# Optimization experiments

Measured on AMD Instinct MI355X. Metric: run time of the kernel, lower is better.

## Reference

```python
import jax, jax.numpy as jnp
import numpy as np

IMAGE_SIZE = 256
CHUNK = 64            # faces per z-buffer scan step
LIGHT = (0.0, 0.0, 3.0)      # PointLights location
AMBIENT, DIFFUSE, SPECULAR, SHININESS = 0.5, 0.3, 0.2, 64.0  # pytorch3d defaults
EPS = 1e-8


def setup_inputs() -> dict:
    n_lat, n_lon, B = 72, 72, 2
    theta = np.linspace(0.15, np.pi - 0.15, n_lat)
    phi = np.linspace(0.0, 2.0 * np.pi, n_lon, endpoint=False)
    t, p = np.meshgrid(theta, phi, indexing='ij')
    sphere = np.stack([np.sin(t) * np.cos(p), np.cos(t), np.sin(t) * np.sin(p)], -1).reshape(-1, 3)
    idx = np.arange(n_lat * n_lon).reshape(n_lat, n_lon)
    idr = np.roll(idx, -1, axis=1)
    f1 = np.stack([idx[:-1], idx[1:], idr[:-1]], -1).reshape(-1, 3)
    f2 = np.stack([idr[:-1], idx[1:], idr[1:]], -1).reshape(-1, 3)
    faces = np.concatenate([f1, f2], 0).astype(np.int32)  # [10224, 3]
    key = jax.random.key(0)
    radii = 1.0 + 0.05 * jax.random.normal(jax.random.fold_in(key, 1), (B, sphere.shape[0], 1))
    vertices = (jnp.asarray(sphere, jnp.float32)[None] * radii).astype(jnp.float32)  # [B,V,3]
    tm = jnp.tile(jnp.eye(4, dtype=jnp.float32)[None], (B, 1, 1)).at[:, 2, 3].set(4.0)  # R=I, T=(0,0,4)
    focal = jnp.full((B, 1), 300.0, jnp.float32)
    pp = jnp.full((1, 2), IMAGE_SIZE / 2.0, jnp.float32)
    return {'vertices': vertices, 'transform_matrix': tm, 'focal_length': focal,
            'principal_point': pp, 'faces': jnp.asarray(faces)}


def _edge(ax, ay, bx, by, px, py):
    return (bx - ax) * (py - ay) - (by - ay) * (px - ax)


def _gather_tri(attr, f_v):
    # attr [B,V,C], f_v [B,P,3] -> [B,P,3,C]
    return jax.vmap(lambda a, f: a[f])(attr, f_v)


def _normalize(v):
    return v / (jnp.linalg.norm(v, axis=-1, keepdims=True) + EPS)


def _rasterize(verts_pix, faces_chunks, px, py):
    # verts_pix [B,V,3] (x_pix, y_pix, z_view); faces_chunks [n_chunks, CHUNK, 3]
    B, P = verts_pix.shape[0], px.shape[0]
    vp = jax.lax.stop_gradient(verts_pix)  # hard rasterization: face ids are non-differentiable

    def body(carry, inp):
        zbuf, fid = carry
        fchunk, off = inp
        tri = vp[:, fchunk]                      # [B,C,3,3]
        x, y, z = tri[..., 0], tri[..., 1], tri[..., 2]   # [B,C,3]
        pxb, pyb = px[None, None], py[None, None]
        w0 = _edge(x[..., 1, None], y[..., 1, None], x[..., 2, None], y[..., 2, None], pxb, pyb)
        w1 = _edge(x[..., 2, None], y[..., 2, None], x[..., 0, None], y[..., 0, None], pxb, pyb)
        w2 = _edge(x[..., 0, None], y[..., 0, None], x[..., 1, None], y[..., 1, None], pxb, pyb)
        denom = w0 + w1 + w2                     # signed twice-area, [B,C,P]
        safe = jnp.where(jnp.abs(denom) > EPS, denom, 1.0)
        b0, b1, b2 = w0 / safe, w1 / safe, w2 / safe
        zint = b0 * z[..., 0, None] + b1 * z[..., 1, None] + b2 * z[..., 2, None]
        inside = (b0 >= 0) & (b1 >= 0) & (b2 >= 0) & (jnp.abs(denom) > EPS) & (zint > 1e-4)
        zc = jnp.where(inside, zint, jnp.inf)    # [B,C,P]
        j = jnp.argmin(zc, axis=1)               # [B,P]
        best_z = jnp.take_along_axis(zc, j[:, None, :], axis=1)[:, 0]
        upd = best_z < zbuf
        zbuf = jnp.where(upd, best_z, zbuf)
        fid = jnp.where(upd, off + j.astype(jnp.int32), fid)
        return (zbuf, fid), None

    n_chunks = faces_chunks.shape[0]
    offs = (jnp.arange(n_chunks) * CHUNK).astype(jnp.int32)
    init = (jnp.full((B, P), jnp.inf, vp.dtype), jnp.zeros((B, P), jnp.int32))
    (zbuf, fid), _ = jax.lax.scan(body, init, (faces_chunks, offs))
    return zbuf, fid


def _render(vertices, transform_matrix, focal_length, principal_point, faces):
    B, V, _ = vertices.shape
    H = W = IMAGE_SIZE
    P = H * W
    R, T = transform_matrix[:, :3, :3], transform_matrix[:, :3, 3]
    # pytorch3d row-vector convention: X_view = X @ R + T
    vview = jnp.einsum('bvi,bij->bvj', vertices, R) + T[:, None]
    z = vview[..., 2]
    x_pix = focal_length * vview[..., 0] / z + principal_point[:, 0][:, None]
    y_pix = focal_length * vview[..., 1] / z + principal_point[:, 1][:, None]
    verts_pix = jnp.stack([x_pix, y_pix, z], -1)                 # [B,V,3]

    gy, gx = jnp.meshgrid(jnp.arange(H) + 0.5, jnp.arange(W) + 0.5, indexing='ij')
    px, py = gx.reshape(-1).astype(vertices.dtype), gy.reshape(-1).astype(vertices.dtype)

    F = faces.shape[0]
    Fpad = ((F + CHUNK - 1) // CHUNK) * CHUNK
    faces_pad = jnp.pad(faces, ((0, Fpad - F), (0, 0)))          # pad = degenerate (0,0,0)
    zbuf, fid = _rasterize(verts_pix, faces_pad.reshape(-1, CHUNK, 3), px, py)
    valid = jnp.isfinite(zbuf)                                   # [B,P]

    # differentiable re-computation of barycentrics for the winning face
    f_v = faces_pad.reshape(-1, 3)[fid]                          # [B,P,3]
    tp = _gather_tri(verts_pix, f_v)                             # [B,P,3,3]
    xk, yk = tp[..., 0], tp[..., 1]
    w0 = _edge(xk[..., 1], yk[..., 1], xk[..., 2], yk[..., 2], px[None], py[None])
    w1 = _edge(xk[..., 2], yk[..., 2], xk[..., 0], yk[..., 0], px[None], py[None])
    w2 = _edge(xk[..., 0], yk[..., 0], xk[..., 1], yk[..., 1], px[None], py[None])
    denom = w0 + w1 + w2
    safe = jnp.where(jnp.abs(denom) > EPS, denom, 1.0)
    bary = jnp.stack([w0, w1, w2], -1) / safe[..., None]         # [B,P,3]

    # area-weighted vertex normals
    tw = vertices[:, faces]                                      # [B,F,3,3]
    fn = jnp.cross(tw[:, :, 1] - tw[:, :, 0], tw[:, :, 2] - tw[:, :, 0])
    vn = jnp.zeros_like(vertices)
    for k in range(3):
        vn = vn.at[:, faces[:, k]].add(fn)
    vn = _normalize(vn)

    pix_pos = jnp.einsum('bpk,bpkc->bpc', bary, _gather_tri(vertices, f_v))
    pix_n = _normalize(jnp.einsum('bpk,bpkc->bpc', bary, _gather_tri(vn, f_v)))

    cam = -jnp.einsum('bj,bij->bi', T, R)                        # camera center in world
    light = jnp.asarray(LIGHT, vertices.dtype)
    L = _normalize(light - pix_pos)
    Vd = _normalize(cam[:, None] - pix_pos)
    ndl = jnp.sum(pix_n * L, -1)
    refl = 2.0 * ndl[..., None] * pix_n - L
    spec = SPECULAR * jnp.maximum(jnp.sum(refl * Vd, -1), 0.0) ** SHININESS * (ndl > 0)
    col = AMBIENT + DIFFUSE * jnp.maximum(ndl, 0.0) + spec       # white texels -> gray shading
    rgb = jnp.where(valid, col, 1.0)                             # white background
    images = jnp.broadcast_to(rgb[:, None], (B, 3, P)).reshape(B, 3, H, W) * 255.0
    alpha = valid.astype(vertices.dtype).reshape(B, 1, H, W)
    return images, alpha


def reference(vertices, transform_matrix, focal_length, principal_point, faces):
    return _render(vertices, transform_matrix, focal_length, principal_point, faces)
```

## Files before the change

kernel.cpp:

```cpp
#include <hip/hip_runtime.h>
#include <math.h>

#define IMG 256
#define PIX (IMG * IMG)
#define SENT 0xFFFFFFFFFFFFFFFFull


__global__ __launch_bounds__(256) void k_transform(
    const float* __restrict__ verts, const float* __restrict__ tm,
    const float* __restrict__ focal, const float* __restrict__ pp,
    float* __restrict__ vp, float* __restrict__ vn,
    unsigned long long* __restrict__ zpk, int B, int V) {
#pragma clang fp contract(off)
    int idx = blockIdx.x * blockDim.x + threadIdx.x;
    int nthreads = gridDim.x * blockDim.x;
    for (int i = idx; i < B * PIX; i += nthreads) zpk[i] = SENT;
    if (idx >= B * V) return;
    int b = idx / V;
    const float* tmb = tm + b * 16;
    float x = verts[idx * 3 + 0];
    float y = verts[idx * 3 + 1];
    float z = verts[idx * 3 + 2];
    float vv[3];
    for (int j = 0; j < 3; ++j) {
        float s = x * tmb[0 * 4 + j] + y * tmb[1 * 4 + j];
        s = s + z * tmb[2 * 4 + j];
        vv[j] = s + tmb[j * 4 + 3];
    }
    float f = focal[b];
    float xp = (f * vv[0]) / vv[2] + pp[0];
    float yp = (f * vv[1]) / vv[2] + pp[1];
    vp[idx * 3 + 0] = xp;
    vp[idx * 3 + 1] = yp;
    vp[idx * 3 + 2] = vv[2];
    vn[idx * 3 + 0] = 0.0f;
    vn[idx * 3 + 1] = 0.0f;
    vn[idx * 3 + 2] = 0.0f;
}

__global__ __launch_bounds__(256) void k_pack(
    const float* __restrict__ verts, const int* __restrict__ faces,
    const float* __restrict__ vp, float* __restrict__ packed,
    float* __restrict__ vn, int B, int F, int FP, int V) {
#pragma clang fp contract(off)
    int idx = blockIdx.x * blockDim.x + threadIdx.x;
    if (idx >= B * FP) return;
    int b = idx / FP;
    int f = idx - b * FP;
    int i0 = 0, i1 = 0, i2 = 0;
    if (f < F) {
        i0 = faces[f * 3 + 0];
        i1 = faces[f * 3 + 1];
        i2 = faces[f * 3 + 2];
    }
    const float* vpb = vp + (size_t)b * V * 3;
    float* pk = packed + (size_t)idx * 9;
    pk[0] = vpb[i0 * 3 + 0]; pk[1] = vpb[i0 * 3 + 1]; pk[2] = vpb[i0 * 3 + 2];
    pk[3] = vpb[i1 * 3 + 0]; pk[4] = vpb[i1 * 3 + 1]; pk[5] = vpb[i1 * 3 + 2];
    pk[6] = vpb[i2 * 3 + 0]; pk[7] = vpb[i2 * 3 + 1]; pk[8] = vpb[i2 * 3 + 2];
    if (f < F) {
        const float* wv = verts + (size_t)b * V * 3;
        float ax = wv[i1 * 3 + 0] - wv[i0 * 3 + 0];
        float ay = wv[i1 * 3 + 1] - wv[i0 * 3 + 1];
        float az = wv[i1 * 3 + 2] - wv[i0 * 3 + 2];
        float bx = wv[i2 * 3 + 0] - wv[i0 * 3 + 0];
        float by = wv[i2 * 3 + 1] - wv[i0 * 3 + 1];
        float bz = wv[i2 * 3 + 2] - wv[i0 * 3 + 2];
        float fnx = ay * bz - az * by;
        float fny = az * bx - ax * bz;
        float fnz = ax * by - ay * bx;
        float* vnb = vn + (size_t)b * V * 3;
        atomicAdd(&vnb[i0 * 3 + 0], fnx);
        atomicAdd(&vnb[i0 * 3 + 1], fny);
        atomicAdd(&vnb[i0 * 3 + 2], fnz);
        atomicAdd(&vnb[i1 * 3 + 0], fnx);
        atomicAdd(&vnb[i1 * 3 + 1], fny);
        atomicAdd(&vnb[i1 * 3 + 2], fnz);
        atomicAdd(&vnb[i2 * 3 + 0], fnx);
        atomicAdd(&vnb[i2 * 3 + 1], fny);
        atomicAdd(&vnb[i2 * 3 + 2], fnz);
    }
}

__global__ __launch_bounds__(256) void k_raster(
    const float* __restrict__ packed,
    unsigned long long* __restrict__ zpk, int FP) {
#pragma clang fp contract(off)
    int b = blockIdx.y;
    int wid = threadIdx.x >> 6;
    int lane = threadIdx.x & 63;
    int f = blockIdx.x * 4 + wid;
    if (f >= FP) return;

    const float* t = packed + ((size_t)b * FP + f) * 9;
    float x0 = t[0], y0 = t[1], z0 = t[2];
    float x1 = t[3], y1 = t[4], z1 = t[5];
    float x2 = t[6], y2 = t[7], z2 = t[8];

    float xmin = fminf(fminf(x0, x1), x2);
    float xmax = fmaxf(fmaxf(x0, x1), x2);
    float ymin = fminf(fminf(y0, y1), y2);
    float ymax = fmaxf(fmaxf(y0, y1), y2);

    int ix0 = (int)floorf(xmin - 0.5f); ix0 = ix0 < 0 ? 0 : ix0;
    int iy0 = (int)floorf(ymin - 0.5f); iy0 = iy0 < 0 ? 0 : iy0;
    int ix1 = (int)ceilf(xmax - 0.5f);  ix1 = ix1 > IMG - 1 ? IMG - 1 : ix1;
    int iy1 = (int)ceilf(ymax - 0.5f);  iy1 = iy1 > IMG - 1 ? IMG - 1 : iy1;
    int w = ix1 - ix0 + 1;
    int h = iy1 - iy0 + 1;
    if (w <= 0 || h <= 0) return;
    int n = w * h;

    unsigned long long* zb = zpk + (size_t)b * PIX;
    for (int i = lane; i < n; i += 64) {
        int iy = (int)((unsigned)i / (unsigned)w);
        int ix = i - iy * w;
        float px = (float)(ix0 + ix) + 0.5f;
        float py = (float)(iy0 + iy) + 0.5f;
        float w0 = (x2 - x1) * (py - y1) - (y2 - y1) * (px - x1);
        float w1 = (x0 - x2) * (py - y2) - (y0 - y2) * (px - x2);
        float w2 = (x1 - x0) * (py - y0) - (y1 - y0) * (px - x0);
        float denom = (w0 + w1) + w2;
        bool dok = fabsf(denom) > 1e-8f;
        float safe = dok ? denom : 1.0f;
        float b0 = w0 / safe;
        float b1 = w1 / safe;
        float b2 = w2 / safe;
        float zint = (b0 * z0 + b1 * z1) + b2 * z2;
        bool inside = (b0 >= 0.0f) && (b1 >= 0.0f) && (b2 >= 0.0f) &&
                      dok && (zint > 1e-4f);
        if (inside) {
            unsigned long long cand =
                ((unsigned long long)__float_as_uint(zint) << 32) |
                (unsigned int)f;
            atomicMin(&zb[(iy0 + iy) * IMG + (ix0 + ix)], cand);
        }
    }
}

__global__ __launch_bounds__(256) void k_shade(
    const float* __restrict__ verts, const int* __restrict__ faces,
    const float* __restrict__ tm, const float* __restrict__ packed,
    const float* __restrict__ vn, const unsigned long long* __restrict__ zpk,
    float* __restrict__ out, int B, int V, int FP) {
#pragma clang fp contract(off)
    int p = blockIdx.x * blockDim.x + threadIdx.x;
    int b = blockIdx.y;
    if (p >= PIX) return;
    size_t imgbase = (size_t)b * 3 * PIX;
    size_t alphabase = (size_t)B * 3 * PIX + (size_t)b * PIX;
    unsigned long long v = zpk[(size_t)b * PIX + p];
    if (v == SENT) {
        out[imgbase + 0 * PIX + p] = 255.0f;
        out[imgbase + 1 * PIX + p] = 255.0f;
        out[imgbase + 2 * PIX + p] = 255.0f;
        out[alphabase + p] = 0.0f;
        return;
    }
    int f = (int)(v & 0xFFFFFFFFull);
    float px = (float)(p & (IMG - 1)) + 0.5f;
    float py = (float)(p >> 8) + 0.5f;
    const float* t = packed + ((size_t)b * FP + f) * 9;
    float x0 = t[0], y0 = t[1];
    float x1 = t[3], y1 = t[4];
    float x2 = t[6], y2 = t[7];
    float w0 = (x2 - x1) * (py - y1) - (y2 - y1) * (px - x1);
    float w1 = (x0 - x2) * (py - y2) - (y0 - y2) * (px - x2);
    float w2 = (x1 - x0) * (py - y0) - (y1 - y0) * (px - x0);
    float denom = (w0 + w1) + w2;
    float safe = (fabsf(denom) > 1e-8f) ? denom : 1.0f;
    float b0 = w0 / safe;
    float b1 = w1 / safe;
    float b2 = w2 / safe;

    int i0 = faces[f * 3 + 0];
    int i1 = faces[f * 3 + 1];
    int i2 = faces[f * 3 + 2];
    const float* wv = verts + (size_t)b * V * 3;
    const float* vnb = vn + (size_t)b * V * 3;

    float a0 = vnb[i0 * 3 + 0], a1 = vnb[i0 * 3 + 1], a2 = vnb[i0 * 3 + 2];
    float c0 = vnb[i1 * 3 + 0], c1 = vnb[i1 * 3 + 1], c2 = vnb[i1 * 3 + 2];
    float d0 = vnb[i2 * 3 + 0], d1 = vnb[i2 * 3 + 1], d2 = vnb[i2 * 3 + 2];
    float na = sqrtf((a0 * a0 + a1 * a1) + a2 * a2) + 1e-8f;
    float nc = sqrtf((c0 * c0 + c1 * c1) + c2 * c2) + 1e-8f;
    float nd = sqrtf((d0 * d0 + d1 * d1) + d2 * d2) + 1e-8f;
    a0 = a0 / na; a1 = a1 / na; a2 = a2 / na;
    c0 = c0 / nc; c1 = c1 / nc; c2 = c2 / nc;
    d0 = d0 / nd; d1 = d1 / nd; d2 = d2 / nd;

    float pos[3], nr[3];
    for (int c = 0; c < 3; ++c) {
        pos[c] = (b0 * wv[i0 * 3 + c] + b1 * wv[i1 * 3 + c]) + b2 * wv[i2 * 3 + c];
    }
    nr[0] = (b0 * a0 + b1 * c0) + b2 * d0;
    nr[1] = (b0 * a1 + b1 * c1) + b2 * d1;
    nr[2] = (b0 * a2 + b1 * c2) + b2 * d2;
    float nl = sqrtf((nr[0] * nr[0] + nr[1] * nr[1]) + nr[2] * nr[2]) + 1e-8f;
    nr[0] = nr[0] / nl; nr[1] = nr[1] / nl; nr[2] = nr[2] / nl;

    const float* tmb = tm + b * 16;
    float T0 = tmb[3], T1 = tmb[7], T2 = tmb[11];
    float cam[3];
    for (int i = 0; i < 3; ++i)
        cam[i] = -((T0 * tmb[i * 4 + 0] + T1 * tmb[i * 4 + 1]) + T2 * tmb[i * 4 + 2]);

    float Lx = 0.0f - pos[0], Ly = 0.0f - pos[1], Lz = 3.0f - pos[2];
    float Ln = sqrtf((Lx * Lx + Ly * Ly) + Lz * Lz) + 1e-8f;
    Lx = Lx / Ln; Ly = Ly / Ln; Lz = Lz / Ln;
    float Vx = cam[0] - pos[0], Vy = cam[1] - pos[1], Vz = cam[2] - pos[2];
    float Vn2 = sqrtf((Vx * Vx + Vy * Vy) + Vz * Vz) + 1e-8f;
    Vx = Vx / Vn2; Vy = Vy / Vn2; Vz = Vz / Vn2;

    float ndl = (nr[0] * Lx + nr[1] * Ly) + nr[2] * Lz;
    float t2 = 2.0f * ndl;
    float rx = (t2 * nr[0]) - Lx;
    float ry = (t2 * nr[1]) - Ly;
    float rz = (t2 * nr[2]) - Lz;
    float rv = (rx * Vx + ry * Vy) + rz * Vz;
    float sp = powf(fmaxf(rv, 0.0f), 64.0f);
    float spec = (0.2f * sp) * ((ndl > 0.0f) ? 1.0f : 0.0f);
    float col = (0.5f + 0.3f * fmaxf(ndl, 0.0f)) + spec;
    col = col * 255.0f;
    out[imgbase + 0 * PIX + p] = col;
    out[imgbase + 1 * PIX + p] = col;
    out[imgbase + 2 * PIX + p] = col;
    out[alphabase + p] = 1.0f;
}

extern "C" void kernel_launch(void* const* d_in, const int* in_sizes, int n_in,
                              void* d_out, int out_size, void* d_ws, size_t ws_size,
                              hipStream_t stream) {
    const float* verts = (const float*)d_in[0];
    const float* tm    = (const float*)d_in[1];
    const float* focal = (const float*)d_in[2];
    const float* pp    = (const float*)d_in[3];
    const int*   faces = (const int*)d_in[4];

    int B = in_sizes[1] / 16;
    int V = in_sizes[0] / (3 * B);
    int F = in_sizes[4] / 3;
    int FP = ((F + 255) / 256) * 256;

    float* out = (float*)d_out;

    float* vp     = (float*)d_ws;
    float* vn     = vp + (size_t)B * V * 3;
    float* packed = vn + (size_t)B * V * 3;
    unsigned long long* zpk =
        (unsigned long long*)(packed + (size_t)B * FP * 9);

    int nv = B * V;
    k_transform<<<dim3((nv + 255) / 256), dim3(256), 0, stream>>>(
        verts, tm, focal, pp, vp, vn, zpk, B, V);
    k_pack<<<dim3((B * FP + 255) / 256), dim3(256), 0, stream>>>(
        verts, faces, vp, packed, vn, B, F, FP, V);
    k_raster<<<dim3(FP / 4, B), dim3(256), 0, stream>>>(packed, zpk, FP);
    k_shade<<<dim3(PIX / 256, B), dim3(256), 0, stream>>>(
        verts, faces, tm, packed, vn, zpk, out, B, V, FP);
}
```

Baseline: 79.59 us.

## Fuse vertex transform, face packing and normal accumulation into raster kernel

Merges the transform, pack and raster kernels into one kernel. Each wavefront transforms its face's three vertices, accumulates the face normal via atomics and writes the packed triangle, then rasterizes it. The z-buffer is inverted so it can be cleared to zero with a single hipMemsetAsync (also zeroing normals), using atomicMax instead of atomicMin. This removes two launches and the intermediate projected-vertex buffer, at the cost of each shared vertex being transformed several times redundantly.

```diff
diff --git a/kernel.cpp b/kernel.cpp
--- a/kernel.cpp
+++ b/kernel.cpp
@@ -3,105 +3,79 @@
 
 #define IMG 256
 #define PIX (IMG * IMG)
-#define SENT 0xFFFFFFFFFFFFFFFFull
-
-
-__global__ __launch_bounds__(256) void k_transform(
-    const float* __restrict__ verts, const float* __restrict__ tm,
-    const float* __restrict__ focal, const float* __restrict__ pp,
-    float* __restrict__ vp, float* __restrict__ vn,
-    unsigned long long* __restrict__ zpk, int B, int V) {
-#pragma clang fp contract(off)
-    int idx = blockIdx.x * blockDim.x + threadIdx.x;
-    int nthreads = gridDim.x * blockDim.x;
-    for (int i = idx; i < B * PIX; i += nthreads) zpk[i] = SENT;
-    if (idx >= B * V) return;
-    int b = idx / V;
-    const float* tmb = tm + b * 16;
-    float x = verts[idx * 3 + 0];
-    float y = verts[idx * 3 + 1];
-    float z = verts[idx * 3 + 2];
-    float vv[3];
-    for (int j = 0; j < 3; ++j) {
-        float s = x * tmb[0 * 4 + j] + y * tmb[1 * 4 + j];
-        s = s + z * tmb[2 * 4 + j];
-        vv[j] = s + tmb[j * 4 + 3];
-    }
-    float f = focal[b];
-    float xp = (f * vv[0]) / vv[2] + pp[0];
-    float yp = (f * vv[1]) / vv[2] + pp[1];
-    vp[idx * 3 + 0] = xp;
-    vp[idx * 3 + 1] = yp;
-    vp[idx * 3 + 2] = vv[2];
-    vn[idx * 3 + 0] = 0.0f;
-    vn[idx * 3 + 1] = 0.0f;
-    vn[idx * 3 + 2] = 0.0f;
-}
-
-__global__ __launch_bounds__(256) void k_pack(
+
+
+__global__ __launch_bounds__(256) void k_fused(
     const float* __restrict__ verts, const int* __restrict__ faces,
-    const float* __restrict__ vp, float* __restrict__ packed,
-    float* __restrict__ vn, int B, int F, int FP, int V) {
-#pragma clang fp contract(off)
-    int idx = blockIdx.x * blockDim.x + threadIdx.x;
-    if (idx >= B * FP) return;
-    int b = idx / FP;
-    int f = idx - b * FP;
-    int i0 = 0, i1 = 0, i2 = 0;
-    if (f < F) {
-        i0 = faces[f * 3 + 0];
-        i1 = faces[f * 3 + 1];
-        i2 = faces[f * 3 + 2];
-    }
-    const float* vpb = vp + (size_t)b * V * 3;
-    float* pk = packed + (size_t)idx * 9;
-    pk[0] = vpb[i0 * 3 + 0]; pk[1] = vpb[i0 * 3 + 1]; pk[2] = vpb[i0 * 3 + 2];
-    pk[3] = vpb[i1 * 3 + 0]; pk[4] = vpb[i1 * 3 + 1]; pk[5] = vpb[i1 * 3 + 2];
-    pk[6] = vpb[i2 * 3 + 0]; pk[7] = vpb[i2 * 3 + 1]; pk[8] = vpb[i2 * 3 + 2];
-    if (f < F) {
-        const float* wv = verts + (size_t)b * V * 3;
-        float ax = wv[i1 * 3 + 0] - wv[i0 * 3 + 0];
-        float ay = wv[i1 * 3 + 1] - wv[i0 * 3 + 1];
-        float az = wv[i1 * 3 + 2] - wv[i0 * 3 + 2];
-        float bx = wv[i2 * 3 + 0] - wv[i0 * 3 + 0];
-        float by = wv[i2 * 3 + 1] - wv[i0 * 3 + 1];
-        float bz = wv[i2 * 3 + 2] - wv[i0 * 3 + 2];
-        float fnx = ay * bz - az * by;
-        float fny = az * bx - ax * bz;
-        float fnz = ax * by - ay * bx;
-        float* vnb = vn + (size_t)b * V * 3;
-        atomicAdd(&vnb[i0 * 3 + 0], fnx);
-        atomicAdd(&vnb[i0 * 3 + 1], fny);
-        atomicAdd(&vnb[i0 * 3 + 2], fnz);
-        atomicAdd(&vnb[i1 * 3 + 0], fnx);
-        atomicAdd(&vnb[i1 * 3 + 1], fny);
-        atomicAdd(&vnb[i1 * 3 + 2], fnz);
-        atomicAdd(&vnb[i2 * 3 + 0], fnx);
-        atomicAdd(&vnb[i2 * 3 + 1], fny);
-        atomicAdd(&vnb[i2 * 3 + 2], fnz);
-    }
-}
-
-__global__ __launch_bounds__(256) void k_raster(
-    const float* __restrict__ packed,
-    unsigned long long* __restrict__ zpk, int FP) {
+    const float* __restrict__ tm, const float* __restrict__ focal,
+    const float* __restrict__ pp, float* __restrict__ packed,
+    float* __restrict__ vn, unsigned long long* __restrict__ zpk,
+    int B, int F, int FP, int V) {
 #pragma clang fp contract(off)
     int b = blockIdx.y;
     int wid = threadIdx.x >> 6;
     int lane = threadIdx.x & 63;
     int f = blockIdx.x * 4 + wid;
-    if (f >= FP) return;
-
-    const float* t = packed + ((size_t)b * FP + f) * 9;
-    float x0 = t[0], y0 = t[1], z0 = t[2];
-    float x1 = t[3], y1 = t[4], z1 = t[5];
-    float x2 = t[6], y2 = t[7], z2 = t[8];
+    if (f >= F) return;
+
+    int i0 = faces[f * 3 + 0];
+    int i1 = faces[f * 3 + 1];
+    int i2 = faces[f * 3 + 2];
+    const float* wv = verts + (size_t)b * V * 3;
+    const float* tmb = tm + b * 16;
+    float fo = focal[b];
+    float ppx = pp[0], ppy = pp[1];
+
+    float w0x = wv[i0 * 3 + 0], w0y = wv[i0 * 3 + 1], w0z = wv[i0 * 3 + 2];
+    float w1x = wv[i1 * 3 + 0], w1y = wv[i1 * 3 + 1], w1z = wv[i1 * 3 + 2];
+    float w2x = wv[i2 * 3 + 0], w2y = wv[i2 * 3 + 1], w2z = wv[i2 * 3 + 2];
+
+#define XFORM(WX, WY, WZ, SX, SY, SZ)                                       \
+    {                                                                       \
+        float s0 = WX * tmb[0] + WY * tmb[4];  s0 = s0 + WZ * tmb[8];       \
+        float v0 = s0 + tmb[3];                                             \
+        float s1 = WX * tmb[1] + WY * tmb[5];  s1 = s1 + WZ * tmb[9];       \
+        float v1 = s1 + tmb[7];                                             \
+        float s2 = WX * tmb[2] + WY * tmb[6];  s2 = s2 + WZ * tmb[10];      \
+        float v2 = s2 + tmb[11];                                            \
+        SX = (fo * v0) / v2 + ppx;                                          \
+        SY = (fo * v1) / v2 + ppy;                                          \
+        SZ = v2;                                                            \
+    }
+    float x0, y0, z0, x1, y1, z1, x2, y2, z2;
+    XFORM(w0x, w0y, w0z, x0, y0, z0)
+    XFORM(w1x, w1y, w1z, x1, y1, z1)
+    XFORM(w2x, w2y, w2z, x2, y2, z2)
+#undef XFORM
+
+    float ax = w1x - w0x, ay = w1y - w0y, az = w1z - w0z;
+    float bx = w2x - w0x, by = w2y - w0y, bz = w2z - w0z;
+    float fnx = ay * bz - az * by;
+    float fny = az * bx - ax * bz;
+    float fnz = ax * by - ay * bx;
+
+    float* vnb = vn + (size_t)b * V * 3;
+    if (lane < 9) {
+        int k = lane / 3;
+        int c = lane - k * 3;
+        int vi = (k == 0) ? i0 : ((k == 1) ? i1 : i2);
+        float val = (c == 0) ? fnx : ((c == 1) ? fny : fnz);
+        atomicAdd(&vnb[vi * 3 + c], val);
+    }
+    float* pk = packed + ((size_t)b * FP + f) * 9;
+    if (lane < 3) {
+        float sx = (lane == 0) ? x0 : ((lane == 1) ? x1 : x2);
+        float sy = (lane == 0) ? y0 : ((lane == 1) ? y1 : y2);
+        float sz = (lane == 0) ? z0 : ((lane == 1) ? z1 : z2);
+        pk[lane * 3 + 0] = sx;
+        pk[lane * 3 + 1] = sy;
+        pk[lane * 3 + 2] = sz;
+    }
 
     float xmin = fminf(fminf(x0, x1), x2);
     float xmax = fmaxf(fmaxf(x0, x1), x2);
     float ymin = fminf(fminf(y0, y1), y2);
     float ymax = fmaxf(fmaxf(y0, y1), y2);
-
     int ix0 = (int)floorf(xmin - 0.5f); ix0 = ix0 < 0 ? 0 : ix0;
     int iy0 = (int)floorf(ymin - 0.5f); iy0 = iy0 < 0 ? 0 : iy0;
     int ix1 = (int)ceilf(xmax - 0.5f);  ix1 = ix1 > IMG - 1 ? IMG - 1 : ix1;
@@ -117,23 +91,23 @@
         int ix = i - iy * w;
         float px = (float)(ix0 + ix) + 0.5f;
         float py = (float)(iy0 + iy) + 0.5f;
-        float w0 = (x2 - x1) * (py - y1) - (y2 - y1) * (px - x1);
-        float w1 = (x0 - x2) * (py - y2) - (y0 - y2) * (px - x2);
-        float w2 = (x1 - x0) * (py - y0) - (y1 - y0) * (px - x0);
-        float denom = (w0 + w1) + w2;
+        float e0 = (x2 - x1) * (py - y1) - (y2 - y1) * (px - x1);
+        float e1 = (x0 - x2) * (py - y2) - (y0 - y2) * (px - x2);
+        float e2 = (x1 - x0) * (py - y0) - (y1 - y0) * (px - x0);
+        float denom = (e0 + e1) + e2;
         bool dok = fabsf(denom) > 1e-8f;
         float safe = dok ? denom : 1.0f;
-        float b0 = w0 / safe;
-        float b1 = w1 / safe;
-        float b2 = w2 / safe;
+        float b0 = e0 / safe;
+        float b1 = e1 / safe;
+        float b2 = e2 / safe;
         float zint = (b0 * z0 + b1 * z1) + b2 * z2;
         bool inside = (b0 >= 0.0f) && (b1 >= 0.0f) && (b2 >= 0.0f) &&
                       dok && (zint > 1e-4f);
         if (inside) {
-            unsigned long long cand =
-                ((unsigned long long)__float_as_uint(zint) << 32) |
-                (unsigned int)f;
-            atomicMin(&zb[(iy0 + iy) * IMG + (ix0 + ix)], cand);
+            unsigned long long key =
+                ~(((unsigned long long)__float_as_uint(zint) << 32) |
+                  (unsigned int)f);
+            atomicMax(&zb[(iy0 + iy) * IMG + (ix0 + ix)], key);
         }
     }
 }
@@ -149,14 +123,15 @@
     if (p >= PIX) return;
     size_t imgbase = (size_t)b * 3 * PIX;
     size_t alphabase = (size_t)B * 3 * PIX + (size_t)b * PIX;
-    unsigned long long v = zpk[(size_t)b * PIX + p];
-    if (v == SENT) {
+    unsigned long long key = zpk[(size_t)b * PIX + p];
+    if (key == 0ull) {
         out[imgbase + 0 * PIX + p] = 255.0f;
         out[imgbase + 1 * PIX + p] = 255.0f;
         out[imgbase + 2 * PIX + p] = 255.0f;
         out[alphabase + p] = 0.0f;
         return;
     }
+    unsigned long long v = ~key;
     int f = (int)(v & 0xFFFFFFFFull);
     float px = (float)(p & (IMG - 1)) + 0.5f;
     float py = (float)(p >> 8) + 0.5f;
@@ -244,18 +219,14 @@
 
     float* out = (float*)d_out;
 
-    float* vp     = (float*)d_ws;
-    float* vn     = vp + (size_t)B * V * 3;
+    unsigned long long* zpk = (unsigned long long*)d_ws;
+    float* vn     = (float*)(zpk + (size_t)B * PIX);
     float* packed = vn + (size_t)B * V * 3;
-    unsigned long long* zpk =
-        (unsigned long long*)(packed + (size_t)B * FP * 9);
-
-    int nv = B * V;
-    k_transform<<<dim3((nv + 255) / 256), dim3(256), 0, stream>>>(
-        verts, tm, focal, pp, vp, vn, zpk, B, V);
-    k_pack<<<dim3((B * FP + 255) / 256), dim3(256), 0, stream>>>(
-        verts, faces, vp, packed, vn, B, F, FP, V);
-    k_raster<<<dim3(FP / 4, B), dim3(256), 0, stream>>>(packed, zpk, FP);
+
+    size_t fill_bytes = (size_t)B * PIX * 8 + (size_t)B * V * 3 * 4;
+    hipMemsetAsync(d_ws, 0, fill_bytes, stream);
+    k_fused<<<dim3(FP / 4, B), dim3(256), 0, stream>>>(
+        verts, faces, tm, focal, pp, packed, vn, zpk, B, F, FP, V);
     k_shade<<<dim3(PIX / 256, B), dim3(256), 0, stream>>>(
         verts, faces, tm, packed, vn, zpk, out, B, V, FP);
 }
```

After: 81.79 us. +2.8%, slower.
